# Kernel tuning notes

Hardware: AMD Instinct MI355X
Metric: run time of the kernel (lower is better)

## Reference

```python
import jax, jax.numpy as jnp
import numpy as np

EPS = 1e-5  # BatchNorm1d default eps
DIMS = [(784, 1024), (1024, 1024), (1024, 1024), (1024, 10)]


def setup_inputs() -> dict:
    key = jax.random.key(0)
    ks = jax.random.split(key, 25)
    d = {"x": jax.random.normal(ks[0], (32768, 784), jnp.float32)}
    for i, (fi, fo) in enumerate(DIMS):
        j = i + 1
        base = 1 + 6 * i
        d[f"W{j}"] = jax.random.uniform(ks[base], (fo, fi), jnp.float32, -1.0, 1.0)
        d[f"b{j}"] = jnp.full((fo,), 0.01, jnp.float32)
        d[f"gamma{j}"] = jax.random.uniform(ks[base + 1], (fo,), jnp.float32, 0.5, 1.5)
        d[f"beta{j}"] = 0.1 * jax.random.normal(ks[base + 2], (fo,), jnp.float32)
        d[f"mean{j}"] = 0.1 * jax.random.normal(ks[base + 3], (fo,), jnp.float32)
        d[f"var{j}"] = jax.random.uniform(ks[base + 4], (fo,), jnp.float32, 0.5, 1.5)
    return d


def _bn(h, gamma, beta, mean, var):
    # inference-mode BatchNorm1d with running stats
    return gamma * (h - mean) * jax.lax.rsqrt(var + EPS) + beta


def reference(x,
              W1, b1, gamma1, beta1, mean1, var1,
              W2, b2, gamma2, beta2, mean2, var2,
              W3, b3, gamma3, beta3, mean3, var3,
              W4, b4, gamma4, beta4, mean4, var4):
    h = x.reshape(-1, 784)
    # layer 1: Quantizer(1) -> BinarizeLinear -> BN -> Hardtanh
    h = jnp.sign(h)
    h = h @ jnp.sign(W1).T + b1
    h = jnp.clip(_bn(h, gamma1, beta1, mean1, var1), -1.0, 1.0)
    # layer 2
    h = jnp.sign(h)
    h = h @ jnp.sign(W2).T + b2
    h = jnp.clip(_bn(h, gamma2, beta2, mean2, var2), -1.0, 1.0)
    # layer 3
    h = jnp.sign(h)
    h = h @ jnp.sign(W3).T + b3
    h = jnp.clip(_bn(h, gamma3, beta3, mean3, var3), -1.0, 1.0)
    # layer 4: Quantizer -> BinarizeLinear -> BN (no hardtanh)
    h = jnp.sign(h)
    h = h @ jnp.sign(W4).T + b4
    return _bn(h, gamma4, beta4, mean4, var4)
```

## Files before the change

kernel.cpp:

```cpp
#include <hip/hip_runtime.h>
#include <cstdint>
#include <climits>


typedef __attribute__((ext_vector_type(4))) int i32x4_t;

__device__ __forceinline__ void gload_lds16(const void* g, void* l) {
  __builtin_amdgcn_global_load_lds(
      (const __attribute__((address_space(1))) unsigned int*)g,
      (__attribute__((address_space(3))) unsigned int*)l, 16, 0, 0);
}

__device__ __forceinline__ int pack4(const float4 v) {
  int b0 = v.x > 0.f ? 1 : (v.x < 0.f ? -1 : 0);
  int b1 = v.y > 0.f ? 1 : (v.y < 0.f ? -1 : 0);
  int b2 = v.z > 0.f ? 1 : (v.z < 0.f ? -1 : 0);
  int b3 = v.w > 0.f ? 1 : (v.w < 0.f ? -1 : 0);
  return (b0 & 0xff) | ((b1 & 0xff) << 8) | ((b2 & 0xff) << 16) | (b3 << 24);
}


__global__ __launch_bounds__(256) void prep_mega_kernel(
    const float* __restrict__ x, int8_t* __restrict__ A0,
    const float* __restrict__ W1f, const float* __restrict__ W2f,
    const float* __restrict__ W3f, const float* __restrict__ W4f,
    int8_t* __restrict__ Wp1, int8_t* __restrict__ Wp2,
    int8_t* __restrict__ Wp3, int8_t* __restrict__ Wp4,
    const float* b1, const float* g1, const float* be1, const float* m1, const float* v1,
    const float* b2, const float* g2, const float* be2, const float* m2, const float* v2,
    const float* b3, const float* g3, const float* be3, const float* m3, const float* v3,
    const float* b4, const float* g4, const float* be4, const float* m4, const float* v4,
    int* __restrict__ T1, int* __restrict__ T2, int* __restrict__ T3,
    int8_t* __restrict__ S1, int8_t* __restrict__ S2, int8_t* __restrict__ S3,
    float* __restrict__ sc4, float* __restrict__ of4) {
  const int b = blockIdx.x;
  const int t = threadIdx.x;
  if (b < 32768) {
    const int col = t * 4;
    if (col < 784) {
      int packed = pack4(*(const float4*)(x + (size_t)b * 784 + col));
      *(int*)(A0 + (size_t)b * 832 + col) = packed;
    } else if (col < 832) {
      *(int*)(A0 + (size_t)b * 832 + col) = 0;
    }
  } else if (b < 35968) {
    const int b2i = b - 32768;
    const float* Wf; int8_t* Wp; int N, K, n, ost;
    if (b2i < 1024)      { Wf = W1f; Wp = Wp1; N = 1024; K = 784;  n = b2i;        ost = 832;  }
    else if (b2i < 2048) { Wf = W2f; Wp = Wp2; N = 1024; K = 1024; n = b2i - 1024; ost = 1024; }
    else if (b2i < 3072) { Wf = W3f; Wp = Wp3; N = 1024; K = 1024; n = b2i - 2048; ost = 1024; }
    else                 { Wf = W4f; Wp = Wp4; N = 10;   K = 1024; n = b2i - 3072; ost = 1024; }
    const int col = t * 4;
    if (col < ost) {
      int packed = 0;
      if (n < N && col + 3 < K)
        packed = pack4(*(const float4*)(Wf + (size_t)n * K + col));
      *(int*)(Wp + (size_t)n * ost + col) = packed;
    }
  } else {
    const int pb = b - 35968;
    if (pb < 12) {
      const int layer = pb >> 2;
      const int n = (pb & 3) * 256 + t;
      const float *bb, *gg, *be, *me, *va; int* T; int8_t* S;
      if (layer == 0)      { bb = b1; gg = g1; be = be1; me = m1; va = v1; T = T1; S = S1; }
      else if (layer == 1) { bb = b2; gg = g2; be = be2; me = m2; va = v2; T = T2; S = S2; }
      else                 { bb = b3; gg = g3; be = be3; me = m3; va = v3; T = T3; S = S3; }
      double g = (double)gg[n];
      double rs = 1.0 / sqrt((double)va[n] + 1e-5);
      int th; int8_t s;
      if (g > 0.0) {
        double tv = (double)me[n] - (double)bb[n] - (double)be[n] / (g * rs);
        tv = fmin(fmax(tv, -2.0e9), 2.0e9);
        th = (int)floor(tv) + 1; s = 1;
      } else if (g < 0.0) {
        double tv = (double)me[n] - (double)bb[n] - (double)be[n] / (g * rs);
        tv = fmin(fmax(tv, -2.0e9), 2.0e9);
        th = (int)ceil(tv); s = -1;
      } else {
        th = INT_MIN; s = (be[n] > 0.f) ? (int8_t)1 : (int8_t)-1;
      }
      T[n] = th; S[n] = s;
    } else if (t < 10) {
      double rs = 1.0 / sqrt((double)v4[t] + 1e-5);
      double sd = (double)g4[t] * rs;
      sc4[t] = (float)sd;
      of4[t] = (float)(sd * ((double)b4[t] - (double)m4[t]) + (double)be4[t]);
    }
  }
}

__global__ __launch_bounds__(256, 2) void gemm_bnn128x256_kernel(
    const int8_t* __restrict__ A, const int8_t* __restrict__ W,
    int ldk, int nkt,
    const int* __restrict__ T, const int8_t* __restrict__ S,
    int8_t* __restrict__ Aout) {
  __shared__ i32x4_t smem[3072];
  int8_t* sm = (int8_t*)smem;
  const int tid = threadIdx.x;
  const int lane = tid & 63;
  const int wn = tid >> 6;

  const int bid = blockIdx.x;
  const int swz = (bid & 7) * 128 + (bid >> 3);
  const int row0 = (swz >> 2) * 128;
  const int col0 = (swz & 3) * 256;

  const int jA0 = tid, jA1 = tid + 256;
  const int rA0 = jA0 >> 2, rA1 = jA1 >> 2;
  const int sA0 = (jA0 & 3) ^ ((rA0 >> 1) & 3);
  const int sA1 = (jA1 & 3) ^ ((rA1 >> 1) & 3);
  const int8_t* aS0 = A + (size_t)(row0 + rA0) * ldk + sA0 * 16;
  const int8_t* aS1 = A + (size_t)(row0 + rA1) * ldk + sA1 * 16;
  const int dA0 = jA0 * 16, dA1 = jA1 * 16;

  const int8_t* bSrc[4];
  int dB[4];
#pragma unroll
  for (int k = 0; k < 4; ++k) {
    const int j = tid + 256 * k;
    const int r = j >> 2;
    const int s = (j & 3) ^ ((r >> 1) & 3);
    bSrc[k] = W + (size_t)(col0 + r) * ldk + s * 16;
    dB[k] = 8192 + j * 16;
  }

  int a_off[8], b_off[4];
#pragma unroll
  for (int m = 0; m < 8; ++m) {
    int ra = m * 16 + (lane & 15);
    a_off[m] = ra * 64 + ((((lane >> 4) ^ (ra >> 1)) & 3) << 4);
  }
#pragma unroll
  for (int n = 0; n < 4; ++n) {
    int rb = wn * 64 + n * 16 + (lane & 15);
    b_off[n] = 8192 + rb * 64 + ((((lane >> 4) ^ (rb >> 1)) & 3) << 4);
  }

  i32x4_t acc[8][4];
#pragma unroll
  for (int m = 0; m < 8; ++m)
#pragma unroll
    for (int n = 0; n < 4; ++n) acc[m][n] = (i32x4_t){0, 0, 0, 0};

  gload_lds16(aS0, sm + dA0);
  gload_lds16(aS1, sm + dA1);
#pragma unroll
  for (int k = 0; k < 4; ++k) gload_lds16(bSrc[k], sm + dB[k]);

  for (int kt = 0; kt < nkt; ++kt) {
    const int nxt = kt + 1;
    const int8_t* const bufr = sm + ((kt & 1) ? 24576 : 0);
    if (nxt < nkt) {
      int8_t* const bufw = sm + ((nxt & 1) ? 24576 : 0);
      aS0 += 64; aS1 += 64;
      gload_lds16(aS0, bufw + dA0);
      gload_lds16(aS1, bufw + dA1);
#pragma unroll
      for (int k = 0; k < 4; ++k) {
        bSrc[k] += 64;
        gload_lds16(bSrc[k], bufw + dB[k]);
      }
      asm volatile("s_waitcnt vmcnt(6)" ::: "memory");
    } else {
      asm volatile("s_waitcnt vmcnt(0)" ::: "memory");
    }
    asm volatile("s_barrier" ::: "memory");

    i32x4_t av[8], bv[4];
#pragma unroll
    for (int i = 0; i < 8; ++i) av[i] = *(const i32x4_t*)(bufr + a_off[i]);
#pragma unroll
    for (int i = 0; i < 4; ++i) bv[i] = *(const i32x4_t*)(bufr + b_off[i]);
    __builtin_amdgcn_s_setprio(1);
#pragma unroll
    for (int m = 0; m < 8; ++m)
#pragma unroll
      for (int n = 0; n < 4; ++n)
        acc[m][n] = __builtin_amdgcn_mfma_i32_16x16x64_i8(av[m], bv[n], acc[m][n], 0, 0, 0);
    __builtin_amdgcn_s_setprio(0);
    asm volatile("s_barrier" ::: "memory");
  }

#pragma unroll
  for (int n = 0; n < 4; ++n) {
    const int oc = col0 + wn * 64 + n * 16 + (lane & 15);
    const int tn = T[oc];
    const int8_t sn = S[oc];
#pragma unroll
    for (int m = 0; m < 8; ++m) {
      const int orb = row0 + m * 16 + ((lane >> 4) << 2);
#pragma unroll
      for (int r = 0; r < 4; ++r) {
        int8_t v = (acc[m][n][r] >= tn) ? sn : (int8_t)(-sn);
        Aout[(size_t)(orb + r) * 1024 + oc] = v;
      }
    }
  }
}

__global__ __launch_bounds__(256) void gemm_final_kernel(
    const int8_t* __restrict__ A, const int8_t* __restrict__ W,
    int ldk, int nkt,
    const float* __restrict__ scale, const float* __restrict__ offs,
    float* __restrict__ out) {
  __shared__ i32x4_t smem[2048];
  int8_t* sm = (int8_t*)smem;
  const int tid = threadIdx.x;
  const int lane = tid & 63;
  const int w = tid >> 6;
  const int wrow = w >> 1, wcol = w & 1;
  const int row0 = blockIdx.x * 128;
  const int col0 = 0;

  const int jj0 = tid, jj1 = tid + 256;
  const int r0 = jj0 >> 2, r1 = jj1 >> 2;
  const int s0 = (jj0 & 3) ^ ((r0 >> 1) & 3);
  const int s1 = (jj1 & 3) ^ ((r1 >> 1) & 3);
  const int8_t* aS0 = A + (size_t)(row0 + r0) * ldk + s0 * 16;
  const int8_t* aS1 = A + (size_t)(row0 + r1) * ldk + s1 * 16;
  const int8_t* bS0 = W + (size_t)(col0 + r0) * ldk + s0 * 16;
  const int8_t* bS1 = W + (size_t)(col0 + r1) * ldk + s1 * 16;
  const int dA0 = jj0 * 16, dA1 = jj1 * 16;
  const int dB0 = 8192 + jj0 * 16, dB1 = 8192 + jj1 * 16;

  int a_off[4], b_off[4];
#pragma unroll
  for (int i = 0; i < 4; ++i) {
    int ra = wrow * 64 + i * 16 + (lane & 15);
    a_off[i] = ra * 64 + ((((lane >> 4) ^ (ra >> 1)) & 3) << 4);
    int rb = wcol * 64 + i * 16 + (lane & 15);
    b_off[i] = 8192 + rb * 64 + ((((lane >> 4) ^ (rb >> 1)) & 3) << 4);
  }

  i32x4_t acc[4][4];
#pragma unroll
  for (int m = 0; m < 4; ++m)
#pragma unroll
    for (int n = 0; n < 4; ++n) acc[m][n] = (i32x4_t){0, 0, 0, 0};

  gload_lds16(aS0, sm + dA0);
  gload_lds16(aS1, sm + dA1);
  gload_lds16(bS0, sm + dB0);
  gload_lds16(bS1, sm + dB1);

  for (int kt = 0; kt < nkt - 1; ++kt) {
    aS0 += 64; aS1 += 64; bS0 += 64; bS1 += 64;
    int8_t* smw = sm + (((kt + 1) & 1) << 14);
    gload_lds16(aS0, smw + dA0);
    gload_lds16(aS1, smw + dA1);
    gload_lds16(bS0, smw + dB0);
    gload_lds16(bS1, smw + dB1);
    asm volatile("s_waitcnt vmcnt(4)" ::: "memory");
    asm volatile("s_barrier" ::: "memory");
    const int8_t* smr = sm + ((kt & 1) << 14);
    i32x4_t av[4], bv[4];
#pragma unroll
    for (int i = 0; i < 4; ++i) av[i] = *(const i32x4_t*)(smr + a_off[i]);
#pragma unroll
    for (int i = 0; i < 4; ++i) bv[i] = *(const i32x4_t*)(smr + b_off[i]);
#pragma unroll
    for (int m = 0; m < 4; ++m)
#pragma unroll
      for (int n = 0; n < 4; ++n)
        acc[m][n] = __builtin_amdgcn_mfma_i32_16x16x64_i8(av[m], bv[n], acc[m][n], 0, 0, 0);
    asm volatile("s_barrier" ::: "memory");
  }
  asm volatile("s_waitcnt vmcnt(0)" ::: "memory");
  asm volatile("s_barrier" ::: "memory");
  {
    const int8_t* smr = sm + (((nkt - 1) & 1) << 14);
    i32x4_t av[4], bv[4];
#pragma unroll
    for (int i = 0; i < 4; ++i) av[i] = *(const i32x4_t*)(smr + a_off[i]);
#pragma unroll
    for (int i = 0; i < 4; ++i) bv[i] = *(const i32x4_t*)(smr + b_off[i]);
#pragma unroll
    for (int m = 0; m < 4; ++m)
#pragma unroll
      for (int n = 0; n < 4; ++n)
        acc[m][n] = __builtin_amdgcn_mfma_i32_16x16x64_i8(av[m], bv[n], acc[m][n], 0, 0, 0);
  }

#pragma unroll
  for (int n = 0; n < 4; ++n) {
    const int oc = col0 + wcol * 64 + n * 16 + (lane & 15);
    if (oc < 10) {
      const float sc = scale[oc], of = offs[oc];
#pragma unroll
      for (int m = 0; m < 4; ++m) {
        const int orb = row0 + wrow * 64 + m * 16 + ((lane >> 4) << 2);
#pragma unroll
        for (int r = 0; r < 4; ++r)
          out[(size_t)(orb + r) * 10 + oc] = sc * (float)acc[m][n][r] + of;
      }
    }
  }
}


#define A0_STRIDE 28

__global__ __launch_bounds__(256) void pack_w_kernel(
    const float* __restrict__ W, uint32_t* __restrict__ Wp,
    int nout, int K, int wstride) {
  int idx = blockIdx.x * blockDim.x + threadIdx.x;
  if (idx >= nout * wstride) return;
  int n = idx / wstride;
  int wi = idx - n * wstride;
  const float* wr = W + (size_t)n * K;
  uint32_t word = 0;
  int base = wi * 32;
  for (int i = 0; i < 32; ++i) {
    int c = base + i;
    if (c < K && wr[c] > 0.f) word |= (1u << i);
  }
  Wp[idx] = word;
}

__global__ __launch_bounds__(256) void prep_thr_kernel(
    const float* __restrict__ b, const float* __restrict__ gamma,
    const float* __restrict__ beta, const float* __restrict__ mean,
    const float* __restrict__ var, int K, int N,
    int* __restrict__ thr, uint32_t* __restrict__ flipm) {
  int n = blockIdx.x * blockDim.x + threadIdx.x;
  if (n >= N) return;
  double g = (double)gamma[n];
  double rs = 1.0 / sqrt((double)var[n] + 1e-5);
  int th;
  if (g != 0.0) {
    double t = (double)mean[n] - (double)b[n] - (double)beta[n] / (g * rs);
    double pt = ((double)K - t) * 0.5;
    th = (g > 0.0) ? (int)ceil(pt) : ((int)floor(pt) + 1);
  } else {
    th = (beta[n] > 0.f) ? (K + 2) : -1;
  }
  thr[n] = th;
  if ((n & 31) == 0) {
    uint32_t m = 0;
    for (int i = 0; i < 32 && (n + i) < N; ++i)
      if (gamma[n + i] < 0.f) m |= (1u << i);
    flipm[n >> 5] = m;
  }
}

__global__ __launch_bounds__(64) void prep_out_kernel(
    const float* __restrict__ b, const float* __restrict__ gamma,
    const float* __restrict__ beta, const float* __restrict__ mean,
    const float* __restrict__ var, int N,
    float* __restrict__ s, float* __restrict__ o) {
  int n = threadIdx.x;
  if (n >= N) return;
  double rs = 1.0 / sqrt((double)var[n] + 1e-5);
  double sd = (double)gamma[n] * rs;
  s[n] = (float)sd;
  o[n] = (float)(sd * ((double)b[n] - (double)mean[n]) + (double)beta[n]);
}

__global__ __launch_bounds__(256) void pack_a_kernel(
    const float* __restrict__ x, uint32_t* __restrict__ A0) {
  int gt = blockIdx.x * blockDim.x + threadIdx.x;
  int wv = gt >> 6;
  int lane = gt & 63;
  int row = wv / 13;
  int seg = wv - row * 13;
  int col = (seg << 6) + lane;
  bool pred = (col < 784) && (x[(size_t)row * 784 + col] > 0.f);
  unsigned long long m = __ballot(pred);
  int widx = seg * 2;
  if (lane == 0)
    A0[(size_t)row * A0_STRIDE + widx] = (uint32_t)m;
  else if (lane == 1 && widx + 1 < 25)
    A0[(size_t)row * A0_STRIDE + widx + 1] = (uint32_t)(m >> 32);
}

__device__ __forceinline__ void layer1024(
    uint32_t a[32], const uint32_t* __restrict__ Wp,
    const int* __restrict__ thr, const uint32_t* __restrict__ fm,
    uint32_t* lds, int lane, int w) {
  const int nb = w * 128;
  uint32_t word = 0;
#pragma unroll 2
  for (int ni = 0; ni < 128; ++ni) {
    const int n = nb + ni;
    const uint32_t* __restrict__ wp = Wp + n * 32;
    uint32_t p0 = 0, p1 = 0, p2 = 0, p3 = 0;
#pragma unroll
    for (int k = 0; k < 32; k += 4) {
      p0 += __popc(a[k + 0] ^ wp[k + 0]);
      p1 += __popc(a[k + 1] ^ wp[k + 1]);
      p2 += __popc(a[k + 2] ^ wp[k + 2]);
      p3 += __popc(a[k + 3] ^ wp[k + 3]);
    }
    int p = (int)(p0 + p1 + p2 + p3);
    word |= ((p < thr[n]) ? 1u : 0u) << (ni & 31);
    if ((ni & 31) == 31) {
      lds[lane * 33 + (n >> 5)] = word ^ fm[n >> 5];
      word = 0;
    }
  }
  __syncthreads();
#pragma unroll
  for (int k = 0; k < 32; ++k) a[k] = lds[lane * 33 + k];
  __syncthreads();
}

__global__ __launch_bounds__(512, 4) void fused_kernel(
    const uint32_t* __restrict__ A0,
    const uint32_t* __restrict__ Wp1, const int* __restrict__ thr1, const uint32_t* __restrict__ fm1,
    const uint32_t* __restrict__ Wp2, const int* __restrict__ thr2, const uint32_t* __restrict__ fm2,
    const uint32_t* __restrict__ Wp3, const int* __restrict__ thr3, const uint32_t* __restrict__ fm3,
    const uint32_t* __restrict__ Wp4, const float* __restrict__ s4, const float* __restrict__ o4,
    float* __restrict__ out) {
  __shared__ uint32_t lds[64 * 33];
  const int lane = threadIdx.x & 63;
  const int w = __builtin_amdgcn_readfirstlane((int)(threadIdx.x >> 6));
  const int row = blockIdx.x * 64 + lane;

  uint32_t a[32];
  {
    const uint4* A4 = (const uint4*)(A0 + (size_t)row * A0_STRIDE);
#pragma unroll
    for (int i = 0; i < 7; ++i) {
      uint4 q = A4[i];
      a[4 * i + 0] = q.x; a[4 * i + 1] = q.y; a[4 * i + 2] = q.z; a[4 * i + 3] = q.w;
    }
  }
  {
    const int nb = w * 128;
    uint32_t word = 0;
#pragma unroll 2
    for (int ni = 0; ni < 128; ++ni) {
      const int n = nb + ni;
      const uint32_t* __restrict__ wp = Wp1 + n * A0_STRIDE;
      uint32_t p0 = 0, p1 = 0, p2 = 0, p3 = 0;
#pragma unroll
      for (int k = 0; k < 24; k += 4) {
        p0 += __popc(a[k + 0] ^ wp[k + 0]);
        p1 += __popc(a[k + 1] ^ wp[k + 1]);
        p2 += __popc(a[k + 2] ^ wp[k + 2]);
        p3 += __popc(a[k + 3] ^ wp[k + 3]);
      }
      p0 += __popc(a[24] ^ wp[24]);
      int p = (int)(p0 + p1 + p2 + p3);
      word |= ((p < thr1[n]) ? 1u : 0u) << (ni & 31);
      if ((ni & 31) == 31) {
        lds[lane * 33 + (n >> 5)] = word ^ fm1[n >> 5];
        word = 0;
      }
    }
    __syncthreads();
#pragma unroll
    for (int k = 0; k < 32; ++k) a[k] = lds[lane * 33 + k];
    __syncthreads();
  }
  layer1024(a, Wp2, thr2, fm2, lds, lane, w);
  layer1024(a, Wp3, thr3, fm3, lds, lane, w);
  for (int j = w; j < 10; j += 8) {
    const uint32_t* __restrict__ wp = Wp4 + j * 32;
    uint32_t p0 = 0, p1 = 0, p2 = 0, p3 = 0;
#pragma unroll
    for (int k = 0; k < 32; k += 4) {
      p0 += __popc(a[k + 0] ^ wp[k + 0]);
      p1 += __popc(a[k + 1] ^ wp[k + 1]);
      p2 += __popc(a[k + 2] ^ wp[k + 2]);
      p3 += __popc(a[k + 3] ^ wp[k + 3]);
    }
    float dotf = 1024.f - 2.f * (float)(p0 + p1 + p2 + p3);
    out[(size_t)row * 10 + j] = s4[j] * dotf + o4[j];
  }
}

extern "C" void kernel_launch(void* const* d_in, const int* in_sizes, int n_in,
                              void* d_out, int out_size, void* d_ws, size_t ws_size,
                              hipStream_t stream) {
  const float* x   = (const float*)d_in[0];
  const float* W1  = (const float*)d_in[1];
  const float* b1  = (const float*)d_in[2];
  const float* g1  = (const float*)d_in[3];
  const float* be1 = (const float*)d_in[4];
  const float* m1  = (const float*)d_in[5];
  const float* v1  = (const float*)d_in[6];
  const float* W2  = (const float*)d_in[7];
  const float* b2  = (const float*)d_in[8];
  const float* g2  = (const float*)d_in[9];
  const float* be2 = (const float*)d_in[10];
  const float* m2  = (const float*)d_in[11];
  const float* v2  = (const float*)d_in[12];
  const float* W3  = (const float*)d_in[13];
  const float* b3  = (const float*)d_in[14];
  const float* g3  = (const float*)d_in[15];
  const float* be3 = (const float*)d_in[16];
  const float* m3  = (const float*)d_in[17];
  const float* v3  = (const float*)d_in[18];
  const float* W4  = (const float*)d_in[19];
  const float* b4  = (const float*)d_in[20];
  const float* g4  = (const float*)d_in[21];
  const float* be4 = (const float*)d_in[22];
  const float* m4  = (const float*)d_in[23];
  const float* v4  = (const float*)d_in[24];
  float* outp = (float*)d_out;
  (void)in_sizes; (void)n_in; (void)out_size;

  uint8_t* ws = (uint8_t*)d_ws;
  const size_t NEED = 100ULL << 20;

  if (ws_size >= NEED) {
    size_t off = 0;
    int8_t* A0  = (int8_t*)(ws + off); off += (size_t)32768 * 832;
    int8_t* Bp1 = (int8_t*)(ws + off); off += (size_t)32768 * 1024;
    int8_t* Bp2 = (int8_t*)(ws + off); off += (size_t)32768 * 1024;
    int8_t* Wp1 = (int8_t*)(ws + off); off += (size_t)1024 * 832;
    int8_t* Wp2 = (int8_t*)(ws + off); off += (size_t)1024 * 1024;
    int8_t* Wp3 = (int8_t*)(ws + off); off += (size_t)1024 * 1024;
    int8_t* Wp4 = (int8_t*)(ws + off); off += (size_t)128 * 1024;
    int* T1     = (int*)(ws + off);    off += 4096;
    int* T2     = (int*)(ws + off);    off += 4096;
    int* T3     = (int*)(ws + off);    off += 4096;
    int8_t* S1  = (int8_t*)(ws + off); off += 1024;
    int8_t* S2  = (int8_t*)(ws + off); off += 1024;
    int8_t* S3  = (int8_t*)(ws + off); off += 1024;
    float* sc4  = (float*)(ws + off);  off += 512;
    float* of4  = (float*)(ws + off);  off += 512;

    prep_mega_kernel<<<35981, 256, 0, stream>>>(
        x, A0, W1, W2, W3, W4, Wp1, Wp2, Wp3, Wp4,
        b1, g1, be1, m1, v1, b2, g2, be2, m2, v2,
        b3, g3, be3, m3, v3, b4, g4, be4, m4, v4,
        T1, T2, T3, S1, S2, S3, sc4, of4);

    gemm_bnn128x256_kernel<<<1024, 256, 0, stream>>>(A0, Wp1, 832, 13, T1, S1, Bp1);
    gemm_bnn128x256_kernel<<<1024, 256, 0, stream>>>(Bp1, Wp2, 1024, 16, T2, S2, Bp2);
    gemm_bnn128x256_kernel<<<1024, 256, 0, stream>>>(Bp2, Wp3, 1024, 16, T3, S3, Bp1);
    gemm_final_kernel<<<256, 256, 0, stream>>>(Bp1, Wp4, 1024, 16, sc4, of4, outp);
  } else {
    size_t off = 0;
    uint32_t* A0  = (uint32_t*)(ws + off); off += (size_t)32768 * A0_STRIDE * 4;
    uint32_t* Wp1 = (uint32_t*)(ws + off); off += (size_t)1024 * A0_STRIDE * 4;
    uint32_t* Wp2 = (uint32_t*)(ws + off); off += (size_t)1024 * 32 * 4;
    uint32_t* Wp3 = (uint32_t*)(ws + off); off += (size_t)1024 * 32 * 4;
    uint32_t* Wp4 = (uint32_t*)(ws + off); off += 4096;
    int* thr1     = (int*)(ws + off);      off += 4096;
    int* thr2     = (int*)(ws + off);      off += 4096;
    int* thr3     = (int*)(ws + off);      off += 4096;
    uint32_t* fm1 = (uint32_t*)(ws + off); off += 128;
    uint32_t* fm2 = (uint32_t*)(ws + off); off += 128;
    uint32_t* fm3 = (uint32_t*)(ws + off); off += 128;
    float* s4o    = (float*)(ws + off);    off += 64;
    float* o4o    = (float*)(ws + off);    off += 64;

    pack_w_kernel<<<(1024 * A0_STRIDE + 255) / 256, 256, 0, stream>>>(W1, Wp1, 1024, 784, A0_STRIDE);
    pack_w_kernel<<<(1024 * 32 + 255) / 256, 256, 0, stream>>>(W2, Wp2, 1024, 1024, 32);
    pack_w_kernel<<<(1024 * 32 + 255) / 256, 256, 0, stream>>>(W3, Wp3, 1024, 1024, 32);
    pack_w_kernel<<<(10 * 32 + 255) / 256, 256, 0, stream>>>(W4, Wp4, 10, 1024, 32);
    prep_thr_kernel<<<4, 256, 0, stream>>>(b1, g1, be1, m1, v1, 784, 1024, thr1, fm1);
    prep_thr_kernel<<<4, 256, 0, stream>>>(b2, g2, be2, m2, v2, 1024, 1024, thr2, fm2);
    prep_thr_kernel<<<4, 256, 0, stream>>>(b3, g3, be3, m3, v3, 1024, 1024, thr3, fm3);
    prep_out_kernel<<<1, 64, 0, stream>>>(b4, g4, be4, m4, v4, 10, s4o, o4o);
    pack_a_kernel<<<(32768 * 13) / 4, 256, 0, stream>>>(x, A0);
    fused_kernel<<<512, 512, 0, stream>>>(A0, Wp1, thr1, fm1, Wp2, thr2, fm2,
                                          Wp3, thr3, fm3, Wp4, s4o, o4o, outp);
  }
}
```

Before: 318.3 us.

## Prepack weights in MFMA fragment order and load B directly to registers

The prep kernel now writes binarized weights in a layout matching the MFMA B-operand fragment order, indexed by k-tile, column block and lane. The GEMM kernels then read B straight from global memory into registers, with double-buffered register prefetch, and skip LDS staging for B. LDS use drops from 48KB to 16KB per block, and the LDS reads and barriers for B go away. The cost is that B global loads are no longer shared through LDS across the block, which adds global/L2 traffic and latency exposure.

```diff
diff --git a/kernel.cpp b/kernel.cpp
--- a/kernel.cpp
+++ b/kernel.cpp
@@ -24,8 +24,8 @@
     const float* __restrict__ x, int8_t* __restrict__ A0,
     const float* __restrict__ W1f, const float* __restrict__ W2f,
     const float* __restrict__ W3f, const float* __restrict__ W4f,
-    int8_t* __restrict__ Wp1, int8_t* __restrict__ Wp2,
-    int8_t* __restrict__ Wp3, int8_t* __restrict__ Wp4,
+    int8_t* __restrict__ Wf1, int8_t* __restrict__ Wf2,
+    int8_t* __restrict__ Wf3, int8_t* __restrict__ Wp4,
     const float* b1, const float* g1, const float* be1, const float* m1, const float* v1,
     const float* b2, const float* g2, const float* be2, const float* m2, const float* v2,
     const float* b3, const float* g3, const float* be3, const float* m3, const float* v3,
@@ -43,22 +43,32 @@
     } else if (col < 832) {
       *(int*)(A0 + (size_t)b * 832 + col) = 0;
     }
-  } else if (b < 35968) {
+  } else if (b < 35648) {
     const int b2i = b - 32768;
-    const float* Wf; int8_t* Wp; int N, K, n, ost;
-    if (b2i < 1024)      { Wf = W1f; Wp = Wp1; N = 1024; K = 784;  n = b2i;        ost = 832;  }
-    else if (b2i < 2048) { Wf = W2f; Wp = Wp2; N = 1024; K = 1024; n = b2i - 1024; ost = 1024; }
-    else if (b2i < 3072) { Wf = W3f; Wp = Wp3; N = 1024; K = 1024; n = b2i - 2048; ost = 1024; }
-    else                 { Wf = W4f; Wp = Wp4; N = 10;   K = 1024; n = b2i - 3072; ost = 1024; }
+    const float* Wf; int8_t* Wo; int Kreal, blk;
+    if (b2i < 832)        { Wf = W1f; Wo = Wf1; Kreal = 784;  blk = b2i;        }
+    else if (b2i < 1856)  { Wf = W2f; Wo = Wf2; Kreal = 1024; blk = b2i - 832;  }
+    else                  { Wf = W3f; Wo = Wf3; Kreal = 1024; blk = b2i - 1856; }
+    const int o = (blk * 256 + t) * 4;
+    const int j  = o & 15;
+    const int l6 = (o >> 4) & 63;
+    const int cb = (o >> 10) & 63;
+    const int kt = o >> 16;
+    const int colw = cb * 16 + (l6 & 15);
+    const int k = kt * 64 + ((l6 >> 4) << 4) + j;
+    int packed = 0;
+    if (k < Kreal)
+      packed = pack4(*(const float4*)(Wf + (size_t)colw * Kreal + k));
+    *(int*)(Wo + o) = packed;
+  } else if (b < 35776) {
+    const int n = b - 35648;
     const int col = t * 4;
-    if (col < ost) {
-      int packed = 0;
-      if (n < N && col + 3 < K)
-        packed = pack4(*(const float4*)(Wf + (size_t)n * K + col));
-      *(int*)(Wp + (size_t)n * ost + col) = packed;
-    }
+    int packed = 0;
+    if (n < 10)
+      packed = pack4(*(const float4*)(W4f + (size_t)n * 1024 + col));
+    *(int*)(Wp4 + (size_t)n * 1024 + col) = packed;
   } else {
-    const int pb = b - 35968;
+    const int pb = b - 35776;
     if (pb < 12) {
       const int layer = pb >> 2;
       const int n = (pb & 3) * 256 + t;
@@ -90,12 +100,12 @@
   }
 }
 
-__global__ __launch_bounds__(256, 2) void gemm_bnn128x256_kernel(
-    const int8_t* __restrict__ A, const int8_t* __restrict__ W,
+__global__ __launch_bounds__(256, 2) void gemm_bd_kernel(
+    const int8_t* __restrict__ A, const int8_t* __restrict__ Wf,
     int ldk, int nkt,
     const int* __restrict__ T, const int8_t* __restrict__ S,
     int8_t* __restrict__ Aout) {
-  __shared__ i32x4_t smem[3072];
+  __shared__ i32x4_t smem[1024];
   int8_t* sm = (int8_t*)smem;
   const int tid = threadIdx.x;
   const int lane = tid & 63;
@@ -114,28 +124,15 @@
   const int8_t* aS1 = A + (size_t)(row0 + rA1) * ldk + sA1 * 16;
   const int dA0 = jA0 * 16, dA1 = jA1 * 16;
 
-  const int8_t* bSrc[4];
-  int dB[4];
-#pragma unroll
-  for (int k = 0; k < 4; ++k) {
-    const int j = tid + 256 * k;
-    const int r = j >> 2;
-    const int s = (j & 3) ^ ((r >> 1) & 3);
-    bSrc[k] = W + (size_t)(col0 + r) * ldk + s * 16;
-    dB[k] = 8192 + j * 16;
-  }
-
-  int a_off[8], b_off[4];
+  const int8_t* const bfp =
+      Wf + ((size_t)((swz & 3) * 16 + wn * 4)) * 1024 + lane * 16;
+
+  int a_off[8];
 #pragma unroll
   for (int m = 0; m < 8; ++m) {
     int ra = m * 16 + (lane & 15);
     a_off[m] = ra * 64 + ((((lane >> 4) ^ (ra >> 1)) & 3) << 4);
   }
-#pragma unroll
-  for (int n = 0; n < 4; ++n) {
-    int rb = wn * 64 + n * 16 + (lane & 15);
-    b_off[n] = 8192 + rb * 64 + ((((lane >> 4) ^ (rb >> 1)) & 3) << 4);
-  }
 
   i32x4_t acc[8][4];
 #pragma unroll
@@ -145,42 +142,48 @@
 
   gload_lds16(aS0, sm + dA0);
   gload_lds16(aS1, sm + dA1);
-#pragma unroll
-  for (int k = 0; k < 4; ++k) gload_lds16(bSrc[k], sm + dB[k]);
-
-  for (int kt = 0; kt < nkt; ++kt) {
-    const int nxt = kt + 1;
-    const int8_t* const bufr = sm + ((kt & 1) ? 24576 : 0);
-    if (nxt < nkt) {
-      int8_t* const bufw = sm + ((nxt & 1) ? 24576 : 0);
-      aS0 += 64; aS1 += 64;
-      gload_lds16(aS0, bufw + dA0);
-      gload_lds16(aS1, bufw + dA1);
-#pragma unroll
-      for (int k = 0; k < 4; ++k) {
-        bSrc[k] += 64;
-        gload_lds16(bSrc[k], bufw + dB[k]);
-      }
-      asm volatile("s_waitcnt vmcnt(6)" ::: "memory");
-    } else {
-      asm volatile("s_waitcnt vmcnt(0)" ::: "memory");
-    }
-    asm volatile("s_barrier" ::: "memory");
-
-    i32x4_t av[8], bv[4];
-#pragma unroll
-    for (int i = 0; i < 8; ++i) av[i] = *(const i32x4_t*)(bufr + a_off[i]);
-#pragma unroll
-    for (int i = 0; i < 4; ++i) bv[i] = *(const i32x4_t*)(bufr + b_off[i]);
-    __builtin_amdgcn_s_setprio(1);
-#pragma unroll
-    for (int m = 0; m < 8; ++m)
-#pragma unroll
-      for (int n = 0; n < 4; ++n)
-        acc[m][n] = __builtin_amdgcn_mfma_i32_16x16x64_i8(av[m], bv[n], acc[m][n], 0, 0, 0);
-    __builtin_amdgcn_s_setprio(0);
-    asm volatile("s_barrier" ::: "memory");
-  }
+  aS0 += 64; aS1 += 64;
+  i32x4_t bvA[4], bvB[4];
+#pragma unroll
+  for (int n = 0; n < 4; ++n) bvA[n] = *(const i32x4_t*)(bfp + n * 1024);
+
+#define GEMM_STEP(KT, BVC, BVN)                                               \
+  {                                                                           \
+    const int kt_ = (KT);                                                     \
+    if (kt_ + 1 < nkt) {                                                      \
+      int8_t* bufw = sm + (((kt_ + 1) & 1) << 13);                            \
+      gload_lds16(aS0, bufw + dA0);                                           \
+      gload_lds16(aS1, bufw + dA1);                                           \
+      aS0 += 64; aS1 += 64;                                                   \
+      _Pragma("unroll")                                                       \
+      for (int n = 0; n < 4; ++n)                                             \
+        BVN[n] = *(const i32x4_t*)(bfp + (size_t)(kt_ + 1) * 65536 + n * 1024); \
+      asm volatile("s_waitcnt vmcnt(6)" ::: "memory");                        \
+    } else {                                                                  \
+      asm volatile("s_waitcnt vmcnt(0)" ::: "memory");                        \
+    }                                                                         \
+    asm volatile("s_barrier" ::: "memory");                                   \
+    const int8_t* bufr = sm + ((kt_ & 1) << 13);                              \
+    i32x4_t av[8];                                                            \
+    _Pragma("unroll")                                                         \
+    for (int i = 0; i < 8; ++i) av[i] = *(const i32x4_t*)(bufr + a_off[i]);   \
+    __builtin_amdgcn_s_setprio(1);                                            \
+    _Pragma("unroll")                                                         \
+    for (int m = 0; m < 8; ++m)                                               \
+      _Pragma("unroll")                                                       \
+      for (int n = 0; n < 4; ++n)                                             \
+        acc[m][n] = __builtin_amdgcn_mfma_i32_16x16x64_i8(av[m], BVC[n], acc[m][n], 0, 0, 0); \
+    __builtin_amdgcn_s_setprio(0);                                            \
+    asm volatile("s_barrier" ::: "memory");                                   \
+  }
+
+  int kt = 0;
+  for (; kt + 2 <= nkt; kt += 2) {
+    GEMM_STEP(kt, bvA, bvB);
+    GEMM_STEP(kt + 1, bvB, bvA);
+  }
+  if (kt < nkt) GEMM_STEP(kt, bvA, bvB);
+#undef GEMM_STEP
 
 #pragma unroll
   for (int n = 0; n < 4; ++n) {
@@ -510,9 +513,9 @@
     int8_t* A0  = (int8_t*)(ws + off); off += (size_t)32768 * 832;
     int8_t* Bp1 = (int8_t*)(ws + off); off += (size_t)32768 * 1024;
     int8_t* Bp2 = (int8_t*)(ws + off); off += (size_t)32768 * 1024;
-    int8_t* Wp1 = (int8_t*)(ws + off); off += (size_t)1024 * 832;
-    int8_t* Wp2 = (int8_t*)(ws + off); off += (size_t)1024 * 1024;
-    int8_t* Wp3 = (int8_t*)(ws + off); off += (size_t)1024 * 1024;
+    int8_t* Wf1 = (int8_t*)(ws + off); off += (size_t)13 * 64 * 1024;
+    int8_t* Wf2 = (int8_t*)(ws + off); off += (size_t)16 * 64 * 1024;
+    int8_t* Wf3 = (int8_t*)(ws + off); off += (size_t)16 * 64 * 1024;
     int8_t* Wp4 = (int8_t*)(ws + off); off += (size_t)128 * 1024;
     int* T1     = (int*)(ws + off);    off += 4096;
     int* T2     = (int*)(ws + off);    off += 4096;
@@ -523,15 +526,15 @@
     float* sc4  = (float*)(ws + off);  off += 512;
     float* of4  = (float*)(ws + off);  off += 512;
 
-    prep_mega_kernel<<<35981, 256, 0, stream>>>(
-        x, A0, W1, W2, W3, W4, Wp1, Wp2, Wp3, Wp4,
+    prep_mega_kernel<<<35789, 256, 0, stream>>>(
+        x, A0, W1, W2, W3, W4, Wf1, Wf2, Wf3, Wp4,
         b1, g1, be1, m1, v1, b2, g2, be2, m2, v2,
         b3, g3, be3, m3, v3, b4, g4, be4, m4, v4,
         T1, T2, T3, S1, S2, S3, sc4, of4);
 
-    gemm_bnn128x256_kernel<<<1024, 256, 0, stream>>>(A0, Wp1, 832, 13, T1, S1, Bp1);
-    gemm_bnn128x256_kernel<<<1024, 256, 0, stream>>>(Bp1, Wp2, 1024, 16, T2, S2, Bp2);
-    gemm_bnn128x256_kernel<<<1024, 256, 0, stream>>>(Bp2, Wp3, 1024, 16, T3, S3, Bp1);
+    gemm_bd_kernel<<<1024, 256, 0, stream>>>(A0, Wf1, 832, 13, T1, S1, Bp1);
+    gemm_bd_kernel<<<1024, 256, 0, stream>>>(Bp1, Wf2, 1024, 16, T2, S2, Bp2);
+    gemm_bd_kernel<<<1024, 256, 0, stream>>>(Bp2, Wf3, 1024, 16, T3, S3, Bp1);
     gemm_final_kernel<<<256, 256, 0, stream>>>(Bp1, Wp4, 1024, 16, sc4, of4, outp);
   } else {
     size_t off = 0;
```

Measured after the change: 308.5 us. 1.03x faster.
